# Kernel tuning notes

Hardware: AMD Instinct MI355X
Metric: run time of the kernel (lower is better)

The kernel has to match this reference:

```python
import jax, jax.numpy as jnp
import numpy as np

HEADSIZE = 64  # per-head feature size (attention dim)
KSIZE, STRIDE, PAD = 3, 1, 1


def setup_inputs() -> dict:
    key = jax.random.key(0)
    k1, k2, k3 = jax.random.split(key, 3)
    B, C, T, H, W = 2, 128, 16, 28, 28
    heads = C // HEADSIZE  # 2
    x = jax.random.normal(k1, (B, C, T, H, W), jnp.float32)
    # learned aggregator query (TokenAggregator, size=1), xavier-normal-ish scale
    q = jax.random.normal(k2, (heads, 1, HEADSIZE), jnp.float32) * (2.0 / (1 + HEADSIZE)) ** 0.5
    # output channel projection (MultiHeadLinear-style, heads=1)
    W_out = jax.random.normal(k3, (C, C), jnp.float32) * (2.0 / (C + C)) ** 0.5
    b_out = jnp.zeros((C,), jnp.float32)
    return {"x": x, "q": q, "W_out": W_out, "b_out": b_out}


def _unfold3d(x, k, s, p):
    # torch unfold-via-identity-conv3d equivalent: [B,C,T,H,W] -> [B,C,k^3,To,Ho,Wo]
    B, C, T, H, W = x.shape
    xp = jnp.pad(x, ((0, 0), (0, 0), (p, p), (p, p), (p, p)))
    To = (T + 2 * p - k) // s + 1
    Ho = (H + 2 * p - k) // s + 1
    Wo = (W + 2 * p - k) // s + 1
    taps = []
    for i in range(k):
        for j in range(k):
            for l in range(k):
                taps.append(xp[:, :, i:i + To * s:s, j:j + Ho * s:s, l:l + Wo * s:s])
    return jnp.stack(taps, axis=2)  # [B, C, K, To, Ho, Wo], K = k^3


def reference(x, q, W_out, b_out):
    patches = _unfold3d(x, KSIZE, STRIDE, PAD)          # [B, C, K, To, Ho, Wo]
    B, C, K, To, Ho, Wo = patches.shape
    hs = HEADSIZE
    heads = C // hs
    # tokenize: per spatial location, K window taps are tokens with C channels
    t = patches.transpose(0, 3, 4, 5, 2, 1)             # [B, To, Ho, Wo, K, C]
    # split_heads(headsize): channel dim C -> (headsize slow, heads fast)
    th = t.reshape(B, To, Ho, Wo, K, hs, heads)         # [..., K, hs, heads]
    scale = hs ** -0.5
    # qkv_aggregate: scale applied to BOTH q and k (effective 1/d), softmax over taps
    logits = jnp.einsum('hoc,btuvkch->btuvhok', q * scale, th * scale)  # [B,To,Ho,Wo,heads,1,K]
    attn = jax.nn.softmax(logits, axis=-1)
    res = jnp.einsum('btuvhok,btuvkch->btuvhoc', attn, th)              # [B,To,Ho,Wo,heads,1,hs]
    # merge_heads: channel order (hs slow, head fast) matches the split ordering
    merged = res[:, :, :, :, :, 0, :].transpose(0, 1, 2, 3, 5, 4).reshape(B, To, Ho, Wo, hs * heads)
    # output channel projection
    y = merged @ W_out.T + b_out                         # [B, To, Ho, Wo, C]
    return y.transpose(0, 4, 1, 2, 3)                    # [B, C, To, Ho, Wo]
```

## Files before the change

### kernel.cpp

```cpp
#include <hip/hip_runtime.h>


#define TT 16
#define HH 28
#define WW 28
#define CC 128
#define SP (TT * HH * WW)
#define NPOS (2 * SP)
#define HS 64
#define KT 27
#define MTS 136

typedef __attribute__((ext_vector_type(8))) short bf16x8;
typedef __attribute__((ext_vector_type(4))) float f32x4;

__device__ __forceinline__ unsigned short bf16_rtne(float f) {
    unsigned u = __float_as_uint(f);
    unsigned r = (u + 0x7FFFu + ((u >> 16) & 1u)) >> 16;
    return (unsigned short)r;
}

__global__ __launch_bounds__(256) void wprep_kernel(
    const float* __restrict__ Wout, unsigned short* __restrict__ Wb)
{
    const int i = blockIdx.x * 256 + threadIdx.x;
    Wb[i] = bf16_rtne(Wout[i]);
}

__global__ __launch_bounds__(256) void qfield_kernel(
    const float* __restrict__ x, const float* __restrict__ q,
    float* __restrict__ s)
{
    __shared__ float sp[16][32];
    const int tid = threadIdx.x;
    const int pl  = tid & 31;
    const int g   = tid >> 5;
    const int p   = blockIdx.x * 32 + pl;
    const int b   = p / SP;
    const int si  = p % SP;
    const float* xb = x + (size_t)b * CC * SP + si;

    float acc0 = 0.f, acc1 = 0.f;
    #pragma unroll
    for (int j = 0; j < 16; ++j) {
        const int c = g * 16 + j;
        const float val = xb[(size_t)c * SP];
        const float qv  = q[(c & 1) * HS + (c >> 1)] * (1.0f / 64.0f);
        if (c & 1) acc1 += qv * val; else acc0 += qv * val;
    }
    sp[g][pl]     = acc0;
    sp[8 + g][pl] = acc1;
    __syncthreads();
    if (tid < 64) {
        const int h = tid >> 5, pp = tid & 31;
        float a = 0.f;
        #pragma unroll
        for (int g2 = 0; g2 < 8; ++g2) a += sp[h * 8 + g2][pp];
        s[h * NPOS + blockIdx.x * 32 + pp] = a;
    }
}

__global__ __launch_bounds__(256) void aweight_kernel(
    const float* __restrict__ s, float* __restrict__ aw)
{
    const int idx = blockIdx.x * 256 + threadIdx.x;
    const int p = idx % SP;
    const int h = (idx / SP) & 1;
    const int b = idx / (2 * SP);
    const int v = p % WW, u = (p / WW) % HH, t = p / (WW * HH);
    const float* sf = s + h * NPOS + b * SP;

    float l[KT], msk[KT];
    #pragma unroll
    for (int k = 0; k < KT; ++k) {
        const int dt = k / 9 - 1, du = (k / 3) % 3 - 1, dv = k % 3 - 1;
        const int tt = t + dt, uu = u + du, vv = v + dv;
        const bool ok = (unsigned)tt < TT && (unsigned)uu < HH && (unsigned)vv < WW;
        l[k]   = ok ? sf[(tt * HH + uu) * WW + vv] : 0.f;
        msk[k] = ok ? 1.f : 0.f;
    }
    float m = l[0];
    #pragma unroll
    for (int k = 1; k < KT; ++k) m = fmaxf(m, l[k]);
    float sum = 0.f;
    #pragma unroll
    for (int k = 0; k < KT; ++k) { l[k] = __expf(l[k] - m); sum += l[k]; }
    const float inv = 1.f / sum;
    float* awp = aw + (size_t)(b * 2 + h) * KT * SP + p;
    #pragma unroll
    for (int k = 0; k < KT; ++k)
        awp[(size_t)k * SP] = l[k] * inv * msk[k];
}

__global__ __launch_bounds__(256) void fusedmp_kernel(
    const float* __restrict__ x, const float* __restrict__ aw,
    const unsigned short* __restrict__ Wb, const float* __restrict__ bout,
    float* __restrict__ out)
{
    __shared__ unsigned short s_mt[32][MTS];

    const int pb  = (blockIdx.x & 7) * 98 + (blockIdx.x >> 3);
    const int b   = pb / (SP / 32);
    const int p0  = (pb % (SP / 32)) * 32;
    const int tid = threadIdx.x;

    #pragma unroll
    for (int it = 0; it < 4; ++it) {
        const int task = it * 256 + tid;
        const int c    = task >> 3;
        const int p4g  = task & 7;
        const int p    = p0 + p4g * 4;
        const int v0   = p % WW;
        const int u    = (p / WW) % HH;
        const int t    = p / (WW * HH);
        const int h    = c & 1;
        const float* xc  = x + (size_t)(b * CC + c) * SP;
        const float* awp = aw + (size_t)(b * 2 + h) * KT * SP + p;
        const int vl = (v0 == 0)  ? 0  : v0 - 1;
        const int vr = (v0 == 24) ? 27 : v0 + 4;

        float4 acc = make_float4(0.f, 0.f, 0.f, 0.f);
        #pragma unroll
        for (int dt = -1; dt <= 1; ++dt) {
            #pragma unroll
            for (int du = -1; du <= 1; ++du) {
                const int tt = t + dt, uu = u + du;
                const bool rok = ((unsigned)tt < TT) && ((unsigned)uu < HH);
                const int rbase = rok ? (tt * HH + uu) * WW : 0;
                const float4 a  = *(const float4*)&xc[rbase + v0];
                const float  xl = xc[rbase + vl];
                const float  xr = xc[rbase + vr];
                const int kb = ((dt + 1) * 3 + (du + 1)) * 3;
                const float4 wm = *(const float4*)&awp[(size_t)(kb + 0) * SP];
                const float4 w0 = *(const float4*)&awp[(size_t)(kb + 1) * SP];
                const float4 wp = *(const float4*)&awp[(size_t)(kb + 2) * SP];
                acc.x += wm.x * xl;  acc.y += wm.y * a.x; acc.z += wm.z * a.y; acc.w += wm.w * a.z;
                acc.x += w0.x * a.x; acc.y += w0.y * a.y; acc.z += w0.z * a.z; acc.w += w0.w * a.w;
                acc.x += wp.x * a.y; acc.y += wp.y * a.z; acc.z += wp.z * a.w; acc.w += wp.w * xr;
            }
        }
        s_mt[p4g * 4 + 0][c] = bf16_rtne(acc.x);
        s_mt[p4g * 4 + 1][c] = bf16_rtne(acc.y);
        s_mt[p4g * 4 + 2][c] = bf16_rtne(acc.z);
        s_mt[p4g * 4 + 3][c] = bf16_rtne(acc.w);
    }
    __syncthreads();

    const int w    = tid >> 6;
    const int lane = tid & 63;
    const int lr   = lane & 15;
    const int lk   = lane >> 4;

    #pragma unroll
    for (int ci2 = 0; ci2 < 2; ++ci2) {
        const int cot = w * 2 + ci2;
        const int cob = cot * 16 + lk * 4;
        f32x4 acc0, acc1;
        #pragma unroll
        for (int r = 0; r < 4; ++r) { acc0[r] = bout[cob + r]; acc1[r] = acc0[r]; }

        #pragma unroll
        for (int ks = 0; ks < 4; ++ks) {
            const bf16x8 aA = *(const bf16x8*)&Wb[(size_t)(cot * 16 + lr) * CC + ks * 32 + lk * 8];
            const bf16x8 b0 = *(const bf16x8*)&s_mt[lr     ][ks * 32 + lk * 8];
            const bf16x8 b1 = *(const bf16x8*)&s_mt[16 + lr][ks * 32 + lk * 8];
            acc0 = __builtin_amdgcn_mfma_f32_16x16x32_bf16(aA, b0, acc0, 0, 0, 0);
            acc1 = __builtin_amdgcn_mfma_f32_16x16x32_bf16(aA, b1, acc1, 0, 0, 0);
        }
        const size_t ob = (size_t)b * CC * SP + p0;
        #pragma unroll
        for (int r = 0; r < 4; ++r) {
            out[ob + (size_t)(cob + r) * SP + lr]      = acc0[r];
            out[ob + (size_t)(cob + r) * SP + 16 + lr] = acc1[r];
        }
    }
}

extern "C" void kernel_launch(void* const* d_in, const int* in_sizes, int n_in,
                              void* d_out, int out_size, void* d_ws, size_t ws_size,
                              hipStream_t stream) {
    const float* x    = (const float*)d_in[0];
    const float* q    = (const float*)d_in[1];
    const float* Wout = (const float*)d_in[2];
    const float* bout = (const float*)d_in[3];
    float* out = (float*)d_out;

    float* s  = (float*)d_ws;
    float* aw = s + NPOS;
    unsigned short* Wb = (unsigned short*)(aw + (size_t)4 * KT * SP);

    wprep_kernel  <<<dim3(CC * CC / 256), dim3(256), 0, stream>>>(Wout, Wb);
    qfield_kernel <<<dim3(NPOS / 32),     dim3(256), 0, stream>>>(x, q, s);
    aweight_kernel<<<dim3(4 * SP / 256),  dim3(256), 0, stream>>>(s, aw);
    fusedmp_kernel<<<dim3(2 * (SP / 32)), dim3(256), 0, stream>>>(x, aw, Wb, bout, out);
}
```

Measured before the change: 50.67 us.

## Reuse attention-weight loads across four channels and fold weight prep into aweight kernel

The mix stage now has each thread accumulate four channels that share the same head, so each attention-weight float4 load is reused four times instead of reloaded per channel. The bf16 conversion of the output projection weights is folded into the attention-weight kernel as extra blocks, removing one kernel launch. The trade-off is higher register pressure from four float4 accumulators and more outstanding x loads per thread.

```diff
diff --git a/kernel.cpp b/kernel.cpp
--- a/kernel.cpp
+++ b/kernel.cpp
@@ -18,13 +18,6 @@
     unsigned u = __float_as_uint(f);
     unsigned r = (u + 0x7FFFu + ((u >> 16) & 1u)) >> 16;
     return (unsigned short)r;
-}
-
-__global__ __launch_bounds__(256) void wprep_kernel(
-    const float* __restrict__ Wout, unsigned short* __restrict__ Wb)
-{
-    const int i = blockIdx.x * 256 + threadIdx.x;
-    Wb[i] = bf16_rtne(Wout[i]);
 }
 
 __global__ __launch_bounds__(256) void qfield_kernel(
@@ -60,9 +53,15 @@
     }
 }
 
-__global__ __launch_bounds__(256) void aweight_kernel(
-    const float* __restrict__ s, float* __restrict__ aw)
+__global__ __launch_bounds__(256) void awwprep_kernel(
+    const float* __restrict__ s, float* __restrict__ aw,
+    const float* __restrict__ Wout, unsigned short* __restrict__ Wb)
 {
+    if (blockIdx.x >= 196) {
+        const int i = (blockIdx.x - 196) * 256 + threadIdx.x;
+        Wb[i] = bf16_rtne(Wout[i]);
+        return;
+    }
     const int idx = blockIdx.x * 256 + threadIdx.x;
     const int p = idx % SP;
     const int h = (idx / SP) & 1;
@@ -104,22 +103,22 @@
     const int p0  = (pb % (SP / 32)) * 32;
     const int tid = threadIdx.x;
 
-    #pragma unroll
-    for (int it = 0; it < 4; ++it) {
-        const int task = it * 256 + tid;
-        const int c    = task >> 3;
-        const int p4g  = task & 7;
-        const int p    = p0 + p4g * 4;
-        const int v0   = p % WW;
-        const int u    = (p / WW) % HH;
-        const int t    = p / (WW * HH);
-        const int h    = c & 1;
-        const float* xc  = x + (size_t)(b * CC + c) * SP;
+    {
+        const int cg  = tid >> 3;
+        const int p4g = tid & 7;
+        const int p   = p0 + p4g * 4;
+        const int v0  = p % WW;
+        const int u   = (p / WW) % HH;
+        const int t   = p / (WW * HH);
+        const int h   = cg & 1;
         const float* awp = aw + (size_t)(b * 2 + h) * KT * SP + p;
+        const float* xc0 = x + (size_t)(b * CC + cg) * SP;
         const int vl = (v0 == 0)  ? 0  : v0 - 1;
         const int vr = (v0 == 24) ? 27 : v0 + 4;
 
-        float4 acc = make_float4(0.f, 0.f, 0.f, 0.f);
+        float4 acc[4] = { make_float4(0.f,0.f,0.f,0.f), make_float4(0.f,0.f,0.f,0.f),
+                          make_float4(0.f,0.f,0.f,0.f), make_float4(0.f,0.f,0.f,0.f) };
+
         #pragma unroll
         for (int dt = -1; dt <= 1; ++dt) {
             #pragma unroll
@@ -127,22 +126,33 @@
                 const int tt = t + dt, uu = u + du;
                 const bool rok = ((unsigned)tt < TT) && ((unsigned)uu < HH);
                 const int rbase = rok ? (tt * HH + uu) * WW : 0;
-                const float4 a  = *(const float4*)&xc[rbase + v0];
-                const float  xl = xc[rbase + vl];
-                const float  xr = xc[rbase + vr];
                 const int kb = ((dt + 1) * 3 + (du + 1)) * 3;
                 const float4 wm = *(const float4*)&awp[(size_t)(kb + 0) * SP];
                 const float4 w0 = *(const float4*)&awp[(size_t)(kb + 1) * SP];
                 const float4 wp = *(const float4*)&awp[(size_t)(kb + 2) * SP];
-                acc.x += wm.x * xl;  acc.y += wm.y * a.x; acc.z += wm.z * a.y; acc.w += wm.w * a.z;
-                acc.x += w0.x * a.x; acc.y += w0.y * a.y; acc.z += w0.z * a.z; acc.w += w0.w * a.w;
-                acc.x += wp.x * a.y; acc.y += wp.y * a.z; acc.z += wp.z * a.w; acc.w += wp.w * xr;
+                #pragma unroll
+                for (int ci = 0; ci < 4; ++ci) {
+                    const float* xc = xc0 + (size_t)(32 * ci) * SP;
+                    const float4 a  = *(const float4*)&xc[rbase + v0];
+                    const float  xl = xc[rbase + vl];
+                    const float  xr = xc[rbase + vr];
+                    acc[ci].x += wm.x * xl;  acc[ci].y += wm.y * a.x;
+                    acc[ci].z += wm.z * a.y; acc[ci].w += wm.w * a.z;
+                    acc[ci].x += w0.x * a.x; acc[ci].y += w0.y * a.y;
+                    acc[ci].z += w0.z * a.z; acc[ci].w += w0.w * a.w;
+                    acc[ci].x += wp.x * a.y; acc[ci].y += wp.y * a.z;
+                    acc[ci].z += wp.z * a.w; acc[ci].w += wp.w * xr;
+                }
             }
         }
-        s_mt[p4g * 4 + 0][c] = bf16_rtne(acc.x);
-        s_mt[p4g * 4 + 1][c] = bf16_rtne(acc.y);
-        s_mt[p4g * 4 + 2][c] = bf16_rtne(acc.z);
-        s_mt[p4g * 4 + 3][c] = bf16_rtne(acc.w);
+        #pragma unroll
+        for (int ci = 0; ci < 4; ++ci) {
+            const int c = cg + 32 * ci;
+            s_mt[p4g * 4 + 0][c] = bf16_rtne(acc[ci].x);
+            s_mt[p4g * 4 + 1][c] = bf16_rtne(acc[ci].y);
+            s_mt[p4g * 4 + 2][c] = bf16_rtne(acc[ci].z);
+            s_mt[p4g * 4 + 3][c] = bf16_rtne(acc[ci].w);
+        }
     }
     __syncthreads();
 
@@ -189,8 +199,7 @@
     float* aw = s + NPOS;
     unsigned short* Wb = (unsigned short*)(aw + (size_t)4 * KT * SP);
 
-    wprep_kernel  <<<dim3(CC * CC / 256), dim3(256), 0, stream>>>(Wout, Wb);
     qfield_kernel <<<dim3(NPOS / 32),     dim3(256), 0, stream>>>(x, q, s);
-    aweight_kernel<<<dim3(4 * SP / 256),  dim3(256), 0, stream>>>(s, aw);
+    awwprep_kernel<<<dim3(196 + 64),      dim3(256), 0, stream>>>(s, aw, Wout, Wb);
     fusedmp_kernel<<<dim3(2 * (SP / 32)), dim3(256), 0, stream>>>(x, aw, Wb, bout, out);
 }
```

New measurement: 48.26 us. 4.8% less time.
